# Performance work log

Measured on AMD Instinct MI355X. Metric: run time of the kernel, lower is better.

Reference implementation:

```python
import jax, jax.numpy as jnp
import numpy as np

HID, NL, NH, DH, FF = 768, 12, 12, 64, 3072
VOCAB, MAXPOS = 30522, 512
T_ELE, T_ROLE = 17, 7
B, L = 16, 256
LN_EPS = 1e-12


def _layernorm(x, g, b):
    mu = x.mean(-1, keepdims=True)
    var = ((x - mu) ** 2).mean(-1, keepdims=True)
    return (x - mu) / jnp.sqrt(var + LN_EPS) * g + b


def _bert(datas, word_emb, pos_emb, type_emb, emb_ln_g, emb_ln_b,
          Wq, bq, Wk, bk, Wv, bv, Wo, bo, ln1_g, ln1_b,
          W1, b1, W2, b2, ln2_g, ln2_b):
    Bv, Lv = datas.shape
    x = word_emb[datas] + pos_emb[:Lv][None] + type_emb[0][None, None]
    x = _layernorm(x, emb_ln_g, emb_ln_b)
    for i in range(NL):  # loop over fixed layer count, not data dims
        q = (x @ Wq[i] + bq[i]).reshape(Bv, Lv, NH, DH)
        k = (x @ Wk[i] + bk[i]).reshape(Bv, Lv, NH, DH)
        v = (x @ Wv[i] + bv[i]).reshape(Bv, Lv, NH, DH)
        att = jax.nn.softmax(jnp.einsum('bqhd,bkhd->bhqk', q, k) / jnp.sqrt(jnp.float32(DH)), axis=-1)
        ctx = jnp.einsum('bhqk,bkhd->bqhd', att, v).reshape(Bv, Lv, HID)
        x = _layernorm(x + ctx @ Wo[i] + bo[i], ln1_g[i], ln1_b[i])
        h = jax.nn.gelu(x @ W1[i] + b1[i], approximate=False)
        x = _layernorm(x + h @ W2[i] + b2[i], ln2_g[i], ln2_b[i])
    return x


def _crf_llh(em, tags, mask, start, end, trans):
    # torchcrf CRF.forward with batch_first=True, reduction='sum'
    Bv, Lv, T = em.shape
    bidx = jnp.arange(Bv)
    em_t = jnp.transpose(em, (1, 0, 2))        # [L,B,T]
    tags_t = tags.T.astype(jnp.int32)          # [L,B]
    mask_t = mask.T.astype(em.dtype)           # [L,B]
    # numerator: score of gold path
    score = start[tags_t[0]] + em_t[0][bidx, tags_t[0]]
    def num_step(s, xs):
        e_t, tg, tp, m = xs
        return s + m * (trans[tp, tg] + e_t[bidx, tg]), None
    score, _ = jax.lax.scan(num_step, score, (em_t[1:], tags_t[1:], tags_t[:-1], mask_t[1:]))
    last_idx = (mask_t.sum(0) - 1).astype(jnp.int32)
    num = score + end[tags[bidx, last_idx]]
    # denominator: forward algorithm (log-sum-exp semiring)
    alpha = start[None] + em_t[0]              # [B,T]
    def den_step(a, xs):
        e_t, m = xs
        nxt = jax.nn.logsumexp(a[:, :, None] + trans[None] + e_t[:, None, :], axis=1)
        return jnp.where(m[:, None] > 0, nxt, a), None
    alpha, _ = jax.lax.scan(den_step, alpha, (em_t[1:], mask_t[1:]))
    den = jax.nn.logsumexp(alpha + end[None], axis=1)
    return jnp.sum(num - den)


def _crf_decode(em, start, end, trans):
    # torchcrf CRF.decode without mask -> full-length Viterbi
    Bv = em.shape[0]
    bidx = jnp.arange(Bv)
    em_t = jnp.transpose(em, (1, 0, 2))        # [L,B,T]
    alpha = start[None] + em_t[0]
    def fwd(a, e_t):
        sc = a[:, :, None] + trans[None]       # [B,T_prev,T_cur]
        return jnp.max(sc, axis=1) + e_t, jnp.argmax(sc, axis=1)
    alpha, hist = jax.lax.scan(fwd, alpha, em_t[1:])   # hist [L-1,B,T]
    last = jnp.argmax(alpha + end[None], axis=1)
    def back(cur, h):
        prev = h[bidx, cur]
        return prev, prev
    _, ys = jax.lax.scan(back, last, hist, reverse=True)  # ys[t] = tag at pos t
    return jnp.concatenate([ys, last[None]], axis=0).T    # [B,L]


def setup_inputs() -> dict:
    key = jax.random.key(0)
    ks = iter(jax.random.split(key, 64))
    n = lambda shape: jax.random.normal(next(ks), shape, dtype=jnp.float32) * 0.02
    inp = {
        'datas': jax.random.randint(next(ks), (B, L), 0, VOCAB, dtype=jnp.int32),
        'ele_labels': jax.random.randint(next(ks), (B, L), 0, T_ELE, dtype=jnp.int32),
        'role_labels': jax.random.randint(next(ks), (B, L), 0, T_ROLE, dtype=jnp.int32),
        'seq_mask': jnp.ones((B, L), dtype=bool),
        'word_emb': n((VOCAB, HID)), 'pos_emb': n((MAXPOS, HID)), 'type_emb': n((2, HID)),
        'emb_ln_g': jnp.ones((HID,)), 'emb_ln_b': jnp.zeros((HID,)),
        'Wq': n((NL, HID, HID)), 'bq': jnp.zeros((NL, HID)),
        'Wk': n((NL, HID, HID)), 'bk': jnp.zeros((NL, HID)),
        'Wv': n((NL, HID, HID)), 'bv': jnp.zeros((NL, HID)),
        'Wo': n((NL, HID, HID)), 'bo': jnp.zeros((NL, HID)),
        'ln1_g': jnp.ones((NL, HID)), 'ln1_b': jnp.zeros((NL, HID)),
        'W1': n((NL, HID, FF)), 'b1': jnp.zeros((NL, FF)),
        'W2': n((NL, FF, HID)), 'b2': jnp.zeros((NL, HID)),
        'ln2_g': jnp.ones((NL, HID)), 'ln2_b': jnp.zeros((NL, HID)),
        'W_ele': n((HID, T_ELE)), 'b_ele': jnp.zeros((T_ELE,)),
        'W_role': n((HID, T_ROLE)), 'b_role': jnp.zeros((T_ROLE,)),
        'ele_start': n((T_ELE,)), 'ele_end': n((T_ELE,)), 'ele_trans': n((T_ELE, T_ELE)),
        'role_start': n((T_ROLE,)), 'role_end': n((T_ROLE,)), 'role_trans': n((T_ROLE, T_ROLE)),
    }
    return inp


def reference(datas, ele_labels, role_labels, seq_mask,
              word_emb, pos_emb, type_emb, emb_ln_g, emb_ln_b,
              Wq, bq, Wk, bk, Wv, bv, Wo, bo, ln1_g, ln1_b,
              W1, b1, W2, b2, ln2_g, ln2_b,
              W_ele, b_ele, W_role, b_role,
              ele_start, ele_end, ele_trans, role_start, role_end, role_trans):
    wemb = _bert(datas, word_emb, pos_emb, type_emb, emb_ln_g, emb_ln_b,
                 Wq, bq, Wk, bk, Wv, bv, Wo, bo, ln1_g, ln1_b,
                 W1, b1, W2, b2, ln2_g, ln2_b)
    ele_em = wemb @ W_ele + b_ele
    role_em = wemb @ W_role + b_role
    mask = seq_mask.astype(jnp.float32)
    ele_llh = _crf_llh(ele_em, ele_labels, mask, ele_start, ele_end, ele_trans)
    role_llh = _crf_llh(role_em, role_labels, mask, role_start, role_end, role_trans)
    loss = -ele_llh - role_llh
    ele_dec = _crf_decode(ele_em, ele_start, ele_end, ele_trans)
    role_dec = _crf_decode(role_em, role_start, role_end, role_trans)
    return loss, ele_dec, role_dec
```

## Files before the change

kernel.cpp:

```cpp
#include <hip/hip_runtime.h>
#include <stdint.h>
#include <math.h>

typedef _Float16 f16;
typedef _Float16 f16x8 __attribute__((ext_vector_type(8)));
typedef float f32x4 __attribute__((ext_vector_type(4)));

#define LO_SCALE 2048.0f
#define INV_LO_SCALE (1.0f/2048.0f)
#define LOG2E 1.4426950408889634f
#define MFMA16(a, b, c) __builtin_amdgcn_mfma_f32_16x16x32_f16(a, b, c, 0, 0, 0)

__device__ __forceinline__ void split1(float x, f16 &hi, f16 &lo) {
    f16 h = (f16)x;
    hi = h;
    lo = (f16)((x - (float)h) * LO_SCALE);
}

__device__ __forceinline__ float fexp2(float x) {
#if __has_builtin(__builtin_amdgcn_exp2f)
    return __builtin_amdgcn_exp2f(x);
#else
    return exp2f(x);
#endif
}
__device__ __forceinline__ float flog2(float x) {
#if __has_builtin(__builtin_amdgcn_logf)
    return __builtin_amdgcn_logf(x);
#else
    return log2f(x);
#endif
}

#define GLOAD16(g, l) __builtin_amdgcn_global_load_lds( \
    (const __attribute__((address_space(1))) void*)(g), \
    (__attribute__((address_space(3))) void*)(l), 16, 0, 0)

#define RAW_BARRIER() do { \
    __builtin_amdgcn_s_barrier(); \
    asm volatile("" ::: "memory"); \
    __builtin_amdgcn_sched_barrier(0); \
} while (0)

__device__ __forceinline__ void swz_decode(int &mi, int &ni)
{
    const int NN = gridDim.y;
    int s = blockIdx.x + blockIdx.y * gridDim.x;
    const int c = s & 7;
    const int idx = s >> 3;
    const int mchunk = gridDim.x >> 3;
    const int md = idx / NN;
    mi = c * mchunk + md;
    ni = idx - md * NN;
}

template<int EPI>
__device__ __forceinline__ void epi_write(float val, int row, int col, int N,
                                          float* __restrict__ C,
                                          f16* __restrict__ Oh, f16* __restrict__ Ol,
                                          f16* __restrict__ X2h, f16* __restrict__ X2l,
                                          f16* __restrict__ X3h, f16* __restrict__ X3l)
{
    if constexpr (EPI == 0) {
        C[(size_t)row * N + col] = val;
    } else if constexpr (EPI == 1) {
        float ge = 0.5f * val * (1.0f + erff(val * 0.70710678118654752440f));
        f16 hi, lo;
        split1(ge, hi, lo);
        size_t o = (size_t)row * N + col;
        Oh[o] = hi;
        Ol[o] = lo;
    } else {
        int sect = col >= 1536 ? 2 : (col >= 768 ? 1 : 0);
        int cc = col - sect * 768;
        int hd = cc >> 6;
        int d = cc & 63;
        int bh = (row >> 8) * 12 + hd;
        int lt = row & 255;
        f16 hi, lo;
        split1(val, hi, lo);
        if (sect == 0) {
            size_t o = ((size_t)bh * 256 + lt) * 64 + d;
            Oh[o] = hi; Ol[o] = lo;
        } else if (sect == 1) {
            size_t o = ((size_t)bh * 256 + lt) * 64 + d;
            X2h[o] = hi; X2l[o] = lo;
        } else {
            size_t o = ((size_t)bh * 64 + d) * 256 + lt;
            X3h[o] = hi; X3l[o] = lo;
        }
    }
}

template<int EPI>
__global__ __launch_bounds__(256, 2)
void gemm128(const f16* __restrict__ Ah, const f16* __restrict__ Al,
             const f16* __restrict__ Bh, const f16* __restrict__ Bl,
             const float* __restrict__ bias, float* __restrict__ C,
             f16* __restrict__ Oh, f16* __restrict__ Ol,
             f16* __restrict__ X2h, f16* __restrict__ X2l,
             f16* __restrict__ X3h, f16* __restrict__ X3l, int K, int N)
{
    __shared__ f16 smem[2][16384];

    int mi, ni;
    swz_decode(mi, ni);
    const int m0 = mi * 128;
    const int n0 = ni * 128;

    const int tid = threadIdx.x;
    const int lane = tid & 63;
    const int w = tid >> 6;
    const int l15 = lane & 15;
    const int lg = lane >> 4;

    f32x4 accm[4][4];
    f32x4 accc[4][4];
#pragma unroll
    for (int i = 0; i < 4; ++i)
#pragma unroll
        for (int j = 0; j < 4; ++j) {
            accm[i][j] = (f32x4){0.f, 0.f, 0.f, 0.f};
            accc[i][j] = (f32x4){0.f, 0.f, 0.f, 0.f};
        }

    const f16* gA0 = Ah + (size_t)(m0 + w * 32 + l15) * K + lg * 8;
    const f16* gA1 = gA0 + 16 * (size_t)K;
    const f16* gAl0 = Al + (size_t)(m0 + w * 32 + l15) * K + lg * 8;
    const f16* gAl1 = gAl0 + 16 * (size_t)K;
    const f16* gB0 = Bh + (size_t)(n0 + w * 32 + l15) * K + lg * 8;
    const f16* gB1 = gB0 + 16 * (size_t)K;
    const f16* gBl0 = Bl + (size_t)(n0 + w * 32 + l15) * K + lg * 8;
    const f16* gBl1 = gBl0 + 16 * (size_t)K;
    const int ldsb0 = w * 1024;
    const int ldsb1 = w * 1024 + 512;

    const int nt = K >> 5;

#define STAGE(buf, k0)                                   \
    {                                                    \
        f16* sb = &smem[buf][0];                         \
        GLOAD16(gA0 + (k0), sb + ldsb0);                 \
        GLOAD16(gA1 + (k0), sb + ldsb1);                 \
        GLOAD16(gAl0 + (k0), sb + 4096 + ldsb0);         \
        GLOAD16(gAl1 + (k0), sb + 4096 + ldsb1);         \
        GLOAD16(gB0 + (k0), sb + 8192 + ldsb0);          \
        GLOAD16(gB1 + (k0), sb + 8192 + ldsb1);          \
        GLOAD16(gBl0 + (k0), sb + 12288 + ldsb0);        \
        GLOAD16(gBl1 + (k0), sb + 12288 + ldsb1);        \
    }

    STAGE(0, 0);

    const int fro = lg * 128 + l15 * 8;
    const int wrg = (w >> 1) * 4;
    const int wcg = (w & 1) * 4;

    int cur = 0;
    for (int t = 0; t < nt; ++t) {
        if (t + 1 < nt) {
            STAGE(cur ^ 1, (t + 1) * 32);
            asm volatile("s_waitcnt vmcnt(8)" ::: "memory");
        } else {
            asm volatile("s_waitcnt vmcnt(0)" ::: "memory");
        }
        RAW_BARRIER();

        const f16* sb = &smem[cur][0];
        f16x8 fbh[4], fbl[4];
#pragma unroll
        for (int ni2 = 0; ni2 < 4; ++ni2) {
            int offb = 8192 + (wcg + ni2) * 512 + fro;
            fbh[ni2] = *(const f16x8*)(sb + offb);
            fbl[ni2] = *(const f16x8*)(sb + offb + 4096);
        }
#pragma unroll
        for (int mi2 = 0; mi2 < 4; ++mi2) {
            int offa = (wrg + mi2) * 512 + fro;
            f16x8 fah = *(const f16x8*)(sb + offa);
            f16x8 fal = *(const f16x8*)(sb + offa + 4096);
            __builtin_amdgcn_s_setprio(1);
#pragma unroll
            for (int ni2 = 0; ni2 < 4; ++ni2) {
                accm[mi2][ni2] = MFMA16(fah, fbh[ni2], accm[mi2][ni2]);
                accc[mi2][ni2] = MFMA16(fah, fbl[ni2], accc[mi2][ni2]);
                accc[mi2][ni2] = MFMA16(fal, fbh[ni2], accc[mi2][ni2]);
            }
            __builtin_amdgcn_s_setprio(0);
        }

        asm volatile("s_waitcnt lgkmcnt(0)" ::: "memory");
        RAW_BARRIER();
        cur ^= 1;
    }
#undef STAGE

    const int wr = (w >> 1) * 64;
    const int wc = (w & 1) * 64;
#pragma unroll
    for (int mi2 = 0; mi2 < 4; ++mi2) {
        int row = m0 + wr + mi2 * 16 + lg * 4;
#pragma unroll
        for (int ni2 = 0; ni2 < 4; ++ni2) {
            int col = n0 + wc + ni2 * 16 + l15;
            float bv = bias[col];
#pragma unroll
            for (int j = 0; j < 4; ++j) {
                float val = accm[mi2][ni2][j] + accc[mi2][ni2][j] * INV_LO_SCALE + bv;
                epi_write<EPI>(val, row + j, col, N, C, Oh, Ol, X2h, X2l, X3h, X3l);
            }
        }
    }
}

template<int EPI>
__global__ __launch_bounds__(256, 3)
void gemm_t64c(const f16* __restrict__ Ah, const f16* __restrict__ Al,
               const f16* __restrict__ Bh, const f16* __restrict__ Bl,
               const float* __restrict__ bias, float* __restrict__ C,
               f16* __restrict__ Oh, f16* __restrict__ Ol,
               f16* __restrict__ X2h, f16* __restrict__ X2l,
               f16* __restrict__ X3h, f16* __restrict__ X3l, int K, int N)
{
    __shared__ f16 smem[2][12288];

    int mi, ni;
    swz_decode(mi, ni);
    const int m0 = mi * 128;
    const int n0 = ni * 64;

    const int tid = threadIdx.x;
    const int lane = tid & 63;
    const int w = tid >> 6;
    const int l15 = lane & 15;
    const int lg = lane >> 4;

    f32x4 accm[4][2];
    f32x4 accc[4][2];
#pragma unroll
    for (int i = 0; i < 4; ++i)
#pragma unroll
        for (int j = 0; j < 2; ++j) {
            accm[i][j] = (f32x4){0.f, 0.f, 0.f, 0.f};
            accc[i][j] = (f32x4){0.f, 0.f, 0.f, 0.f};
        }

    const f16* gA0 = Ah + (size_t)(m0 + w * 32 + l15) * K + lg * 8;
    const f16* gA1 = gA0 + 16 * (size_t)K;
    const f16* gAl0 = Al + (size_t)(m0 + w * 32 + l15) * K + lg * 8;
    const f16* gAl1 = gAl0 + 16 * (size_t)K;
    const f16* gB0 = Bh + (size_t)(n0 + w * 16 + l15) * K + lg * 8;
    const f16* gBl0 = Bl + (size_t)(n0 + w * 16 + l15) * K + lg * 8;

    const int nt = K >> 5;

#define STAGEB(buf, k0)                                  \
    {                                                    \
        f16* sb = &smem[buf][0];                         \
        GLOAD16(gA0 + (k0), sb + w * 1024);              \
        GLOAD16(gA1 + (k0), sb + w * 1024 + 512);        \
        GLOAD16(gAl0 + (k0), sb + 4096 + w * 1024);      \
        GLOAD16(gAl1 + (k0), sb + 4096 + w * 1024 + 512);\
        GLOAD16(gB0 + (k0), sb + 8192 + w * 512);        \
        GLOAD16(gBl0 + (k0), sb + 10240 + w * 512);      \
    }

    STAGEB(0, 0);

    const int fro = lg * 128 + l15 * 8;
    const int wrg = (w >> 1) * 4;
    const int wcg = (w & 1) * 2;

    int cur = 0;
    for (int t = 0; t < nt; ++t) {
        if (t + 1 < nt) {
            STAGEB(cur ^ 1, (t + 1) * 32);
            asm volatile("s_waitcnt vmcnt(6)" ::: "memory");
        } else {
            asm volatile("s_waitcnt vmcnt(0)" ::: "memory");
        }
        RAW_BARRIER();

        const f16* sb = &smem[cur][0];
        f16x8 fbh[2], fbl[2];
#pragma unroll
        for (int ni2 = 0; ni2 < 2; ++ni2) {
            int offb = 8192 + (wcg + ni2) * 512 + fro;
            fbh[ni2] = *(const f16x8*)(sb + offb);
            fbl[ni2] = *(const f16x8*)(sb + offb + 2048);
        }
#pragma unroll
        for (int mi2 = 0; mi2 < 4; ++mi2) {
            int offa = (wrg + mi2) * 512 + fro;
            f16x8 fah = *(const f16x8*)(sb + offa);
            f16x8 fal = *(const f16x8*)(sb + offa + 4096);
            __builtin_amdgcn_s_setprio(1);
#pragma unroll
            for (int ni2 = 0; ni2 < 2; ++ni2) {
                accm[mi2][ni2] = MFMA16(fah, fbh[ni2], accm[mi2][ni2]);
                accc[mi2][ni2] = MFMA16(fah, fbl[ni2], accc[mi2][ni2]);
                accc[mi2][ni2] = MFMA16(fal, fbh[ni2], accc[mi2][ni2]);
            }
            __builtin_amdgcn_s_setprio(0);
        }

        asm volatile("s_waitcnt lgkmcnt(0)" ::: "memory");
        RAW_BARRIER();
        cur ^= 1;
    }
#undef STAGEB

    const int wr = (w >> 1) * 64;
    const int wc = (w & 1) * 32;
#pragma unroll
    for (int mi2 = 0; mi2 < 4; ++mi2) {
        int row = m0 + wr + mi2 * 16 + lg * 4;
#pragma unroll
        for (int ni2 = 0; ni2 < 2; ++ni2) {
            int col = n0 + wc + ni2 * 16 + l15;
            float bv = bias[col];
#pragma unroll
            for (int j = 0; j < 4; ++j) {
                float val = accm[mi2][ni2][j] + accc[mi2][ni2][j] * INV_LO_SCALE + bv;
                epi_write<EPI>(val, row + j, col, N, C, Oh, Ol, X2h, X2l, X3h, X3l);
            }
        }
    }
}

__global__ __launch_bounds__(256, 1)
void attn_mfma_kernel(const f16* __restrict__ Qh, const f16* __restrict__ Ql,
                      const f16* __restrict__ Kh, const f16* __restrict__ Kl,
                      const f16* __restrict__ Vth, const f16* __restrict__ Vtl,
                      f16* __restrict__ ch, f16* __restrict__ cl)
{
    __shared__ f16 sKh[256 * 72];
    __shared__ f16 sKl[256 * 72];
    __shared__ f16 sVh[64 * 264];
    __shared__ f16 sVl[64 * 264];
    __shared__ f16 sPh[4][1280];
    __shared__ f16 sPl[4][1280];

    const int bh = blockIdx.x >> 1;
    const int qbase = (blockIdx.x & 1) * 128;
    const int b = bh / 12;
    const int h = bh % 12;
    const int tid = threadIdx.x;
    const int w = tid >> 6;
    const int l = tid & 63;
    const int l15 = l & 15;
    const int lg = l >> 4;

    {
        const f16* gKh = Kh + (size_t)bh * 16384;
        const f16* gKl = Kl + (size_t)bh * 16384;
#pragma unroll
        for (int i = 0; i < 8; ++i) {
            int c = tid + i * 256;
            int off = (c >> 3) * 72 + (c & 7) * 8;
            *(f16x8*)(sKh + off) = *(const f16x8*)(gKh + c * 8);
            *(f16x8*)(sKl + off) = *(const f16x8*)(gKl + c * 8);
        }
        const f16* gVh = Vth + (size_t)bh * 16384;
        const f16* gVl = Vtl + (size_t)bh * 16384;
#pragma unroll
        for (int i = 0; i < 8; ++i) {
            int c = tid + i * 256;
            int off = (c >> 5) * 264 + (c & 31) * 8;
            *(f16x8*)(sVh + off) = *(const f16x8*)(gVh + c * 8);
            *(f16x8*)(sVl + off) = *(const f16x8*)(gVl + c * 8);
        }
    }
    __syncthreads();

    f16x8 qfh[2][2], qfl[2][2];
#pragma unroll
    for (int mt = 0; mt < 2; ++mt) {
        int qr = qbase + w * 32 + mt * 16 + l15;
        size_t qo = ((size_t)bh * 256 + qr) * 64 + lg * 8;
        qfh[mt][0] = *(const f16x8*)(Qh + qo);
        qfh[mt][1] = *(const f16x8*)(Qh + qo + 32);
        qfl[mt][0] = *(const f16x8*)(Ql + qo);
        qfl[mt][1] = *(const f16x8*)(Ql + qo + 32);
    }

    f32x4 S[2][16];
#pragma unroll
    for (int nt = 0; nt < 16; ++nt) {
        int kr = nt * 16 + l15;
        int kaddr = kr * 72 + lg * 8;
        f16x8 kh0 = *(const f16x8*)(sKh + kaddr);
        f16x8 kh1 = *(const f16x8*)(sKh + kaddr + 32);
        f16x8 kl0 = *(const f16x8*)(sKl + kaddr);
        f16x8 kl1 = *(const f16x8*)(sKl + kaddr + 32);
#pragma unroll
        for (int mt = 0; mt < 2; ++mt) {
            f32x4 am = (f32x4){0.f, 0.f, 0.f, 0.f};
            f32x4 ac = (f32x4){0.f, 0.f, 0.f, 0.f};
            am = MFMA16(qfh[mt][0], kh0, am);
            am = MFMA16(qfh[mt][1], kh1, am);
            ac = MFMA16(qfh[mt][0], kl0, ac);
            ac = MFMA16(qfh[mt][1], kl1, ac);
            ac = MFMA16(qfl[mt][0], kh0, ac);
            ac = MFMA16(qfl[mt][1], kh1, ac);
            S[mt][nt] = (am + ac * INV_LO_SCALE) * 0.125f;
        }
    }

#pragma unroll
    for (int mt = 0; mt < 2; ++mt)
#pragma unroll
        for (int j = 0; j < 4; ++j) {
            float m = S[mt][0][j];
#pragma unroll
            for (int nt = 1; nt < 16; ++nt) m = fmaxf(m, S[mt][nt][j]);
            m = fmaxf(m, __shfl_xor(m, 1));
            m = fmaxf(m, __shfl_xor(m, 2));
            m = fmaxf(m, __shfl_xor(m, 4));
            m = fmaxf(m, __shfl_xor(m, 8));
            float s = 0.f;
#pragma unroll
            for (int nt = 0; nt < 16; ++nt) {
                float e = fexp2((S[mt][nt][j] - m) * LOG2E);
                S[mt][nt][j] = e;
                s += e;
            }
            s += __shfl_xor(s, 1);
            s += __shfl_xor(s, 2);
            s += __shfl_xor(s, 4);
            s += __shfl_xor(s, 8);
            float inv = 1.0f / s;
#pragma unroll
            for (int nt = 0; nt < 16; ++nt) S[mt][nt][j] *= inv;
        }

    f32x4 Ohh[2][4], Occ[2][4];
#pragma unroll
    for (int mt = 0; mt < 2; ++mt)
#pragma unroll
        for (int dt = 0; dt < 4; ++dt) {
            Ohh[mt][dt] = (f32x4){0.f, 0.f, 0.f, 0.f};
            Occ[mt][dt] = (f32x4){0.f, 0.f, 0.f, 0.f};
        }

    f16* pbh = &sPh[w][0];
    f16* pbl = &sPl[w][0];
#pragma unroll
    for (int kp = 0; kp < 8; ++kp) {
#pragma unroll
        for (int mt = 0; mt < 2; ++mt)
#pragma unroll
            for (int n2 = 0; n2 < 2; ++n2) {
                int nt = kp * 2 + n2;
#pragma unroll
                for (int j = 0; j < 4; ++j) {
                    int prow = mt * 16 + lg * 4 + j;
                    int pcol = n2 * 16 + l15;
                    f16 hi, lo;
                    split1(S[mt][nt][j], hi, lo);
                    pbh[prow * 40 + pcol] = hi;
                    pbl[prow * 40 + pcol] = lo;
                }
            }
        __builtin_amdgcn_wave_barrier();
#pragma unroll
        for (int mt = 0; mt < 2; ++mt) {
            int paddr = (mt * 16 + l15) * 40 + lg * 8;
            f16x8 ph = *(const f16x8*)(pbh + paddr);
            f16x8 pl = *(const f16x8*)(pbl + paddr);
#pragma unroll
            for (int dt = 0; dt < 4; ++dt) {
                int vaddr = (dt * 16 + l15) * 264 + kp * 32 + lg * 8;
                f16x8 vh = *(const f16x8*)(sVh + vaddr);
                f16x8 vl = *(const f16x8*)(sVl + vaddr);
                Ohh[mt][dt] = MFMA16(ph, vh, Ohh[mt][dt]);
                Occ[mt][dt] = MFMA16(ph, vl, Occ[mt][dt]);
                Occ[mt][dt] = MFMA16(pl, vh, Occ[mt][dt]);
            }
        }
        __builtin_amdgcn_wave_barrier();
    }

#pragma unroll
    for (int mt = 0; mt < 2; ++mt)
#pragma unroll
        for (int dt = 0; dt < 4; ++dt) {
            f32x4 o = Ohh[mt][dt] + Occ[mt][dt] * INV_LO_SCALE;
#pragma unroll
            for (int j = 0; j < 4; ++j) {
                int q = qbase + w * 32 + mt * 16 + lg * 4 + j;
                int d = dt * 16 + l15;
                size_t off = ((size_t)(b * 256 + q)) * 768 + h * 64 + d;
                f16 hi, lo;
                split1(o[j], hi, lo);
                ch[off] = hi;
                cl[off] = lo;
            }
        }
}

__device__ __forceinline__ void tsplit_tile(const float* __restrict__ W,
                                            f16* __restrict__ Th, f16* __restrict__ Tl,
                                            int K, int N, int kb, int nb, int tid,
                                            float (*tile)[33])
{
    const int k0 = kb * 32;
    const int n0 = nb * 32;
    const int r = tid >> 3;
    const int c4 = (tid & 7) * 4;
    float4 v = *(const float4*)&W[(size_t)(k0 + r) * N + n0 + c4];
    tile[r][c4 + 0] = v.x; tile[r][c4 + 1] = v.y;
    tile[r][c4 + 2] = v.z; tile[r][c4 + 3] = v.w;
    __syncthreads();
    f16 hs[4], ls[4];
#pragma unroll
    for (int j = 0; j < 4; ++j) split1(tile[c4 + j][r], hs[j], ls[j]);
    size_t o = (size_t)(n0 + r) * K + k0 + c4;
    Th[o + 0] = hs[0]; Th[o + 1] = hs[1]; Th[o + 2] = hs[2]; Th[o + 3] = hs[3];
    Tl[o + 0] = ls[0]; Tl[o + 1] = ls[1]; Tl[o + 2] = ls[2]; Tl[o + 3] = ls[3];
}

__global__ void tsplit_all_kernel(const float* __restrict__ Wq, const float* __restrict__ Wk,
                                  const float* __restrict__ Wv, const float* __restrict__ Wo,
                                  const float* __restrict__ W1, const float* __restrict__ W2,
                                  f16* __restrict__ qkvh, f16* __restrict__ qkvl,
                                  f16* __restrict__ woh, f16* __restrict__ wol,
                                  f16* __restrict__ w1h, f16* __restrict__ w1l,
                                  f16* __restrict__ w2h, f16* __restrict__ w2l)
{
    __shared__ float tile[32][33];
    const int tid = threadIdx.x;
    int bid = blockIdx.x;
    if (bid < 576) {
        tsplit_tile(Wq, qkvh, qkvl, 768, 768, bid % 24, bid / 24, tid, tile);
    } else if (bid < 1152) {
        bid -= 576;
        tsplit_tile(Wk, qkvh + 768 * 768, qkvl + 768 * 768, 768, 768, bid % 24, bid / 24, tid, tile);
    } else if (bid < 1728) {
        bid -= 1152;
        tsplit_tile(Wv, qkvh + 2 * 768 * 768, qkvl + 2 * 768 * 768, 768, 768, bid % 24, bid / 24, tid, tile);
    } else if (bid < 2304) {
        bid -= 1728;
        tsplit_tile(Wo, woh, wol, 768, 768, bid % 24, bid / 24, tid, tile);
    } else if (bid < 4608) {
        bid -= 2304;
        tsplit_tile(W1, w1h, w1l, 768, 3072, bid % 24, bid / 24, tid, tile);
    } else {
        bid -= 4608;
        tsplit_tile(W2, w2h, w2l, 3072, 768, bid % 96, bid / 96, tid, tile);
    }
}

__global__ void pack_qkv_bias_kernel(const float* __restrict__ bq, const float* __restrict__ bk,
                                     const float* __restrict__ bv, float* __restrict__ qkvb)
{
    const int i = blockIdx.x;
    const int tid = threadIdx.x;
    for (int c = tid; c < 768; c += 256) {
        qkvb[i * 2304 + c]        = bq[i * 768 + c];
        qkvb[i * 2304 + 768 + c]  = bk[i * 768 + c];
        qkvb[i * 2304 + 1536 + c] = bv[i * 768 + c];
    }
}

__device__ void ln_emit(float* vals, float* red, const float* __restrict__ g,
                        const float* __restrict__ be, float* xout,
                        f16* oh, f16* ol, size_t base, int tid)
{
    float s = vals[tid] + vals[tid + 256] + vals[tid + 512];
    red[tid] = s;
    __syncthreads();
    for (int st = 128; st > 0; st >>= 1) { if (tid < st) red[tid] += red[tid + st]; __syncthreads(); }
    float mu = red[0] * (1.0f / 768.0f);
    __syncthreads();
    float d0 = vals[tid] - mu, d1 = vals[tid + 256] - mu, d2 = vals[tid + 512] - mu;
    red[tid] = d0 * d0 + d1 * d1 + d2 * d2;
    __syncthreads();
    for (int st = 128; st > 0; st >>= 1) { if (tid < st) red[tid] += red[tid + st]; __syncthreads(); }
    float var = red[0] * (1.0f / 768.0f);
    float rstd = 1.0f / sqrtf(var + 1e-12f);
    __syncthreads();
    for (int c = tid; c < 768; c += 256) {
        float o = (vals[c] - mu) * rstd * g[c] + be[c];
        if (xout) xout[base + c] = o;
        f16 hi, lo;
        split1(o, hi, lo);
        oh[base + c] = hi;
        ol[base + c] = lo;
    }
}

__global__ void embed_ln_kernel(const int* __restrict__ datas, const float* __restrict__ wemb,
                                const float* __restrict__ pemb, const float* __restrict__ temb,
                                const float* __restrict__ g, const float* __restrict__ be,
                                float* __restrict__ x, f16* __restrict__ xh, f16* __restrict__ xl)
{
    __shared__ float vals[768];
    __shared__ float red[256];
    const int i = blockIdx.x;
    const int tid = threadIdx.x;
    const int l = i & 255;
    const int widx = datas[i];
    for (int c = tid; c < 768; c += 256)
        vals[c] = wemb[(size_t)widx * 768 + c] + pemb[(size_t)l * 768 + c] + temb[c];
    __syncthreads();
    ln_emit(vals, red, g, be, x, xh, xl, (size_t)i * 768, tid);
}

__global__ void res_ln_kernel(float* __restrict__ x, const float* __restrict__ y,
                              const float* __restrict__ g, const float* __restrict__ be,
                              f16* __restrict__ xh, f16* __restrict__ xl)
{
    __shared__ float vals[768];
    __shared__ float red[256];
    const int i = blockIdx.x;
    const int tid = threadIdx.x;
    const size_t base = (size_t)i * 768;
    for (int c = tid; c < 768; c += 256) vals[c] = x[base + c] + y[base + c];
    __syncthreads();
    ln_emit(vals, red, g, be, x, xh, xl, base, tid);
}

__global__ void head_kernel(const float* __restrict__ X, const float* __restrict__ Wh,
                            const float* __restrict__ bh, float* __restrict__ out, int T)
{
    __shared__ float xs[768];
    __shared__ double part[8][32];
    const int i = blockIdx.x;
    const int tid = threadIdx.x;
    for (int c = tid; c < 768; c += 256) xs[c] = X[(size_t)i * 768 + c];
    __syncthreads();
    const int p = tid >> 5;
    const int tg = tid & 31;
    if (tg < T) {
        double a = 0;
        for (int d = p * 96; d < p * 96 + 96; ++d)
            a += (double)xs[d] * (double)Wh[d * T + tg];
        part[p][tg] = a;
    }
    __syncthreads();
    if (tid < T) {
        double s = 0;
        for (int pp = 0; pp < 8; ++pp) s += part[pp][tid];
        out[(size_t)i * T + tid] = (float)(s + (double)bh[tid]);
    }
}

__global__ void crf_num_kernel(const float* __restrict__ em, const int* __restrict__ labels,
                               const float* __restrict__ start, const float* __restrict__ endv,
                               const float* __restrict__ trans, float* __restrict__ num, int T)
{
    __shared__ double red[256];
    const int b = blockIdx.x;
    const int tid = threadIdx.x;
    const int tag = labels[b * 256 + tid];
    float v;
    if (tid == 0) {
        v = start[tag] + em[(size_t)(b * 256) * T + tag];
    } else {
        int pt = labels[b * 256 + tid - 1];
        v = trans[pt * T + tag] + em[(size_t)(b * 256 + tid) * T + tag];
    }
    red[tid] = (double)v;
    __syncthreads();
    for (int st = 128; st > 0; st >>= 1) { if (tid < st) red[tid] += red[tid + st]; __syncthreads(); }
    if (tid == 0) num[b] = (float)(red[0] + (double)endv[labels[b * 256 + 255]]);
}

template<int T>
__global__ void crf_scan_kernel(const float* __restrict__ emG, const float* __restrict__ start,
                                const float* __restrict__ endv, const float* __restrict__ trans,
                                float* __restrict__ den, float* __restrict__ tagOut)
{
    __shared__ float ems[256 * T];
    __shared__ float albuf[32];
    __shared__ unsigned char hist[255 * T + 1];
    const int b = blockIdx.x;
    const bool vit = (blockIdx.y == 1);
    const int c = threadIdx.x;

    for (int idx = c; idx < 256 * T; idx += 64)
        ems[idx] = emG[(size_t)b * 256 * T + idx];
    float trc[T];
#pragma unroll
    for (int p = 0; p < T; ++p) trc[p] = (c < T) ? trans[p * T + c] : 0.f;
    const float ec = (c < T) ? endv[c] : -1e30f;
    __syncthreads();

    float alpha = (c < T) ? (start[c] + ems[c]) : -1e30f;

    if (!vit) {
        for (int t = 1; t < 256; ++t) {
            if (c < T) albuf[c] = alpha;
            __builtin_amdgcn_wave_barrier();
            float a[T];
            float m = -1e30f;
#pragma unroll
            for (int p = 0; p < T; ++p) { a[p] = albuf[p] + trc[p]; m = fmaxf(m, a[p]); }
            float s = 0.f;
#pragma unroll
            for (int p = 0; p < T; ++p) s += fexp2((a[p] - m) * LOG2E);
            float na = m + flog2(s) * 0.6931471805599453f + ems[t * T + c];
            __builtin_amdgcn_wave_barrier();
            if (c < T) alpha = na;
        }
        if (c < T) albuf[c] = alpha + ec;
        __builtin_amdgcn_wave_barrier();
        if (c == 0) {
            float m = -1e30f;
            for (int p = 0; p < T; ++p) m = fmaxf(m, albuf[p]);
            float s = 0.f;
            for (int p = 0; p < T; ++p) s += fexp2((albuf[p] - m) * LOG2E);
            den[b] = m + flog2(s) * 0.6931471805599453f;
        }
    } else {
        for (int t = 1; t < 256; ++t) {
            if (c < T) albuf[c] = alpha;
            __builtin_amdgcn_wave_barrier();
            float best = albuf[0] + trc[0];
            int arg = 0;
#pragma unroll
            for (int p = 1; p < T; ++p) {
                float v2 = albuf[p] + trc[p];
                if (v2 > best) { best = v2; arg = p; }
            }
            __builtin_amdgcn_wave_barrier();
            if (c < T) {
                alpha = best + ems[t * T + c];
                hist[(t - 1) * T + c] = (unsigned char)arg;
            }
        }
        if (c < T) albuf[c] = alpha + ec;
        __builtin_amdgcn_wave_barrier();
        if (c == 0) {
            float bv = albuf[0];
            int cur = 0;
            for (int p = 1; p < T; ++p) {
                if (albuf[p] > bv) { bv = albuf[p]; cur = p; }
            }
            tagOut[b * 256 + 255] = (float)cur;
            for (int t = 254; t >= 0; --t) {
                cur = hist[t * T + cur];
                tagOut[b * 256 + t] = (float)cur;
            }
        }
    }
}

__global__ void loss_kernel(const float* __restrict__ num, const float* __restrict__ den,
                            float* __restrict__ out)
{
    __shared__ double red[32];
    const int tid = threadIdx.x;
    red[tid] = (double)num[tid] - (double)den[tid];
    __syncthreads();
    for (int st = 16; st > 0; st >>= 1) { if (tid < st) red[tid] += red[tid + st]; __syncthreads(); }
    if (tid == 0) out[0] = (float)(-red[0]);
}

extern "C" void kernel_launch(void* const* d_in, const int* in_sizes, int n_in,
                              void* d_out, int out_size, void* d_ws, size_t ws_size,
                              hipStream_t stream)
{
    (void)in_sizes; (void)n_in; (void)out_size; (void)ws_size;
    const int* datas       = (const int*)d_in[0];
    const int* ele_labels  = (const int*)d_in[1];
    const int* role_labels = (const int*)d_in[2];
    const float* word_emb = (const float*)d_in[4];
    const float* pos_emb  = (const float*)d_in[5];
    const float* type_emb = (const float*)d_in[6];
    const float* emb_g = (const float*)d_in[7];
    const float* emb_b = (const float*)d_in[8];
    const float* Wq = (const float*)d_in[9];  const float* bq = (const float*)d_in[10];
    const float* Wk = (const float*)d_in[11]; const float* bk = (const float*)d_in[12];
    const float* Wv = (const float*)d_in[13]; const float* bv = (const float*)d_in[14];
    const float* Wo = (const float*)d_in[15]; const float* bo = (const float*)d_in[16];
    const float* ln1g = (const float*)d_in[17]; const float* ln1b = (const float*)d_in[18];
    const float* W1 = (const float*)d_in[19]; const float* b1 = (const float*)d_in[20];
    const float* W2 = (const float*)d_in[21]; const float* b2 = (const float*)d_in[22];
    const float* ln2g = (const float*)d_in[23]; const float* ln2b = (const float*)d_in[24];
    const float* W_ele = (const float*)d_in[25]; const float* b_ele = (const float*)d_in[26];
    const float* W_role = (const float*)d_in[27]; const float* b_role = (const float*)d_in[28];
    const float* ele_start = (const float*)d_in[29];
    const float* ele_end   = (const float*)d_in[30];
    const float* ele_trans = (const float*)d_in[31];
    const float* role_start = (const float*)d_in[32];
    const float* role_end   = (const float*)d_in[33];
    const float* role_trans = (const float*)d_in[34];
    float* out = (float*)d_out;

    uint8_t* ws = (uint8_t*)d_ws;
    float* x      = (float*)(ws + 0x0000000);
    f16* xh       = (f16*)  (ws + 0x0C00000);
    f16* xl       = (f16*)  (ws + 0x1200000);
    f16* Qh       = (f16*)  (ws + 0x1800000);
    f16* Ql       = (f16*)  (ws + 0x1E00000);
    f16* Kh       = (f16*)  (ws + 0x2400000);
    f16* Kl       = (f16*)  (ws + 0x2A00000);
    f16* Vth      = (f16*)  (ws + 0x3000000);
    f16* Vtl      = (f16*)  (ws + 0x3600000);
    f16* ctxh     = (f16*)  (ws + 0x3C00000);
    f16* ctxl     = (f16*)  (ws + 0x4200000);
    float* rbuf   = (float*)(ws + 0x4800000);
    f16* hh       = (f16*)  (ws + 0x1800000);
    f16* hl       = (f16*)  (ws + 0x3000000);
    f16* wqkv_h   = (f16*)  (ws + 0x5400000);
    f16* wqkv_l   = (f16*)  (ws + 0x5760000);
    f16* wo_h     = (f16*)  (ws + 0x5AC0000);
    f16* wo_l     = (f16*)  (ws + 0x5BE0000);
    f16* w1_h     = (f16*)  (ws + 0x5D00000);
    f16* w1_l     = (f16*)  (ws + 0x6180000);
    f16* w2_h     = (f16*)  (ws + 0x6600000);
    f16* w2_l     = (f16*)  (ws + 0x6A80000);
    float* qkvb   = (float*)(ws + 0x6F00000);
    float* ele_em = (float*)(ws + 0x6F20000);
    float* role_em= (float*)(ws + 0x6F70000);
    float* numb   = (float*)(ws + 0x6FC0000);
    float* denb   = (float*)(ws + 0x6FC0100);

    pack_qkv_bias_kernel<<<12, 256, 0, stream>>>(bq, bk, bv, qkvb);
    embed_ln_kernel<<<4096, 256, 0, stream>>>(datas, word_emb, pos_emb, type_emb,
                                              emb_g, emb_b, x, xh, xl);

    for (int i = 0; i < 12; ++i) {
        const size_t o768 = (size_t)i * 768 * 768;
        const size_t o3072 = (size_t)i * 768 * 3072;
        tsplit_all_kernel<<<6912, 256, 0, stream>>>(Wq + o768, Wk + o768, Wv + o768, Wo + o768,
                                                    W1 + o3072, W2 + o3072,
                                                    wqkv_h, wqkv_l, wo_h, wo_l,
                                                    w1_h, w1_l, w2_h, w2_l);
        gemm128<2><<<dim3(32, 18), 256, 0, stream>>>(xh, xl, wqkv_h, wqkv_l,
                                                     qkvb + i * 2304, nullptr,
                                                     Qh, Ql, Kh, Kl, Vth, Vtl, 768, 2304);
        attn_mfma_kernel<<<384, 256, 0, stream>>>(Qh, Ql, Kh, Kl, Vth, Vtl, ctxh, ctxl);
        gemm_t64c<0><<<dim3(32, 12), 256, 0, stream>>>(ctxh, ctxl, wo_h, wo_l,
                                                       bo + i * 768, rbuf, nullptr, nullptr,
                                                       nullptr, nullptr, nullptr, nullptr, 768, 768);
        res_ln_kernel<<<4096, 256, 0, stream>>>(x, rbuf, ln1g + i * 768, ln1b + i * 768, xh, xl);
        gemm128<1><<<dim3(32, 24), 256, 0, stream>>>(xh, xl, w1_h, w1_l,
                                                     b1 + i * 3072, nullptr, hh, hl,
                                                     nullptr, nullptr, nullptr, nullptr, 768, 3072);
        gemm_t64c<0><<<dim3(32, 12), 256, 0, stream>>>(hh, hl, w2_h, w2_l,
                                                       b2 + i * 768, rbuf, nullptr, nullptr,
                                                       nullptr, nullptr, nullptr, nullptr, 3072, 768);
        res_ln_kernel<<<4096, 256, 0, stream>>>(x, rbuf, ln2g + i * 768, ln2b + i * 768, xh, xl);
    }

    head_kernel<<<4096, 256, 0, stream>>>(x, W_ele, b_ele, ele_em, 17);
    head_kernel<<<4096, 256, 0, stream>>>(x, W_role, b_role, role_em, 7);

    crf_num_kernel<<<16, 256, 0, stream>>>(ele_em, ele_labels, ele_start, ele_end, ele_trans, numb, 17);
    crf_num_kernel<<<16, 256, 0, stream>>>(role_em, role_labels, role_start, role_end, role_trans, numb + 16, 7);
    crf_scan_kernel<17><<<dim3(16, 2), 64, 0, stream>>>(ele_em, ele_start, ele_end, ele_trans, denb, out + 1);
    crf_scan_kernel<7><<<dim3(16, 2), 64, 0, stream>>>(role_em, role_start, role_end, role_trans, denb + 16, out + 1 + 4096);
    loss_kernel<<<1, 32, 0, stream>>>(numb, denb, out);
}
```

Measured before the change: 5.826 ms.

## Replace 128x128 GEMM with 256x128 8-wave triple-buffered interleaved-load kernel

Replaces the 4-wave 128x128 double-buffered GEMM used for the QKV and FFN1 projections with an 8-wave 256x128 tile kernel. It uses a three-stage LDS ring, prefetching two K-steps ahead, and spreads the global-to-LDS stage loads across the MFMA sub-iterations with per-subtile barriers. The aim is better latency hiding and more reuse of each B tile. In exchange it uses more LDS and allows only one block per CU. It also halves the grid, which may leave CUs underfilled on a 256-CU part, and adds many more barriers.

```diff
diff --git a/kernel.cpp b/kernel.cpp
--- a/kernel.cpp
+++ b/kernel.cpp
@@ -93,20 +93,20 @@
 }
 
 template<int EPI>
-__global__ __launch_bounds__(256, 2)
-void gemm128(const f16* __restrict__ Ah, const f16* __restrict__ Al,
-             const f16* __restrict__ Bh, const f16* __restrict__ Bl,
-             const float* __restrict__ bias, float* __restrict__ C,
-             f16* __restrict__ Oh, f16* __restrict__ Ol,
-             f16* __restrict__ X2h, f16* __restrict__ X2l,
-             f16* __restrict__ X3h, f16* __restrict__ X3l, int K, int N)
-{
-    __shared__ f16 smem[2][16384];
-
-    int mi, ni;
-    swz_decode(mi, ni);
-    const int m0 = mi * 128;
-    const int n0 = ni * 128;
+__global__ __launch_bounds__(512, 1)
+void gemm8p(const f16* __restrict__ Ah, const f16* __restrict__ Al,
+            const f16* __restrict__ Bh, const f16* __restrict__ Bl,
+            const float* __restrict__ bias, float* __restrict__ C,
+            f16* __restrict__ Oh, f16* __restrict__ Ol,
+            f16* __restrict__ X2h, f16* __restrict__ X2l,
+            f16* __restrict__ X3h, f16* __restrict__ X3l, int K, int N)
+{
+    __shared__ f16 smem[3][24576];
+
+    int mi_, ni_;
+    swz_decode(mi_, ni_);
+    const int m0 = mi_ * 256;
+    const int n0 = ni_ * 128;
 
     const int tid = threadIdx.x;
     const int lane = tid & 63;
@@ -128,72 +128,80 @@
     const f16* gA1 = gA0 + 16 * (size_t)K;
     const f16* gAl0 = Al + (size_t)(m0 + w * 32 + l15) * K + lg * 8;
     const f16* gAl1 = gAl0 + 16 * (size_t)K;
-    const f16* gB0 = Bh + (size_t)(n0 + w * 32 + l15) * K + lg * 8;
-    const f16* gB1 = gB0 + 16 * (size_t)K;
-    const f16* gBl0 = Bl + (size_t)(n0 + w * 32 + l15) * K + lg * 8;
-    const f16* gBl1 = gBl0 + 16 * (size_t)K;
-    const int ldsb0 = w * 1024;
-    const int ldsb1 = w * 1024 + 512;
+    const f16* gB0 = Bh + (size_t)(n0 + w * 16 + l15) * K + lg * 8;
+    const f16* gBl0 = Bl + (size_t)(n0 + w * 16 + l15) * K + lg * 8;
 
     const int nt = K >> 5;
 
-#define STAGE(buf, k0)                                   \
-    {                                                    \
-        f16* sb = &smem[buf][0];                         \
-        GLOAD16(gA0 + (k0), sb + ldsb0);                 \
-        GLOAD16(gA1 + (k0), sb + ldsb1);                 \
-        GLOAD16(gAl0 + (k0), sb + 4096 + ldsb0);         \
-        GLOAD16(gAl1 + (k0), sb + 4096 + ldsb1);         \
-        GLOAD16(gB0 + (k0), sb + 8192 + ldsb0);          \
-        GLOAD16(gB1 + (k0), sb + 8192 + ldsb1);          \
-        GLOAD16(gBl0 + (k0), sb + 12288 + ldsb0);        \
-        GLOAD16(gBl1 + (k0), sb + 12288 + ldsb1);        \
-    }
-
-    STAGE(0, 0);
+#define SA_HI(buf, k0) { f16* sb = &smem[buf][0]; \
+    GLOAD16(gA0 + (k0), sb + w * 1024); \
+    GLOAD16(gA1 + (k0), sb + w * 1024 + 512); }
+#define SA_LO(buf, k0) { f16* sb = &smem[buf][0]; \
+    GLOAD16(gAl0 + (k0), sb + 8192 + w * 1024); \
+    GLOAD16(gAl1 + (k0), sb + 8192 + w * 1024 + 512); }
+#define SB_HL(buf, k0) { f16* sb = &smem[buf][0]; \
+    GLOAD16(gB0 + (k0), sb + 16384 + w * 512); \
+    GLOAD16(gBl0 + (k0), sb + 20480 + w * 512); }
+
+    SA_HI(0, 0); SA_LO(0, 0); SB_HL(0, 0);
+    if (nt > 1) { SA_HI(1, 32); SA_LO(1, 32); SB_HL(1, 32); }
 
     const int fro = lg * 128 + l15 * 8;
-    const int wrg = (w >> 1) * 4;
-    const int wcg = (w & 1) * 4;
-
-    int cur = 0;
+    const int wag = (w >> 1) * 4;
+    const int wbg = (w & 1) * 4;
+
+    int bt = 0;
     for (int t = 0; t < nt; ++t) {
         if (t + 1 < nt) {
-            STAGE(cur ^ 1, (t + 1) * 32);
-            asm volatile("s_waitcnt vmcnt(8)" ::: "memory");
+            asm volatile("s_waitcnt vmcnt(6)" ::: "memory");
         } else {
             asm volatile("s_waitcnt vmcnt(0)" ::: "memory");
         }
         RAW_BARRIER();
 
-        const f16* sb = &smem[cur][0];
+        const f16* sb = &smem[bt][0];
+        int bs = bt + 2; if (bs >= 3) bs -= 3;
+        const bool doStage = (t + 2 < nt);
+        const int k2 = (t + 2) * 32;
+
         f16x8 fbh[4], fbl[4];
 #pragma unroll
-        for (int ni2 = 0; ni2 < 4; ++ni2) {
-            int offb = 8192 + (wcg + ni2) * 512 + fro;
-            fbh[ni2] = *(const f16x8*)(sb + offb);
-            fbl[ni2] = *(const f16x8*)(sb + offb + 4096);
-        }
-#pragma unroll
-        for (int mi2 = 0; mi2 < 4; ++mi2) {
-            int offa = (wrg + mi2) * 512 + fro;
+        for (int mt = 0; mt < 4; ++mt) {
+            if (doStage) {
+                if (mt == 0) { SA_HI(bs, k2); }
+                else if (mt == 1) { SA_LO(bs, k2); }
+                else if (mt == 2) { SB_HL(bs, k2); }
+            }
+            if (mt == 0) {
+#pragma unroll
+                for (int ni2 = 0; ni2 < 4; ++ni2) {
+                    int offb = 16384 + (wbg + ni2) * 512 + fro;
+                    fbh[ni2] = *(const f16x8*)(sb + offb);
+                    fbl[ni2] = *(const f16x8*)(sb + offb + 4096);
+                }
+            }
+            int offa = (wag + mt) * 512 + fro;
             f16x8 fah = *(const f16x8*)(sb + offa);
-            f16x8 fal = *(const f16x8*)(sb + offa + 4096);
+            f16x8 fal = *(const f16x8*)(sb + offa + 8192);
+
+            __builtin_amdgcn_s_barrier();
+            asm volatile("s_waitcnt lgkmcnt(0)" ::: "memory");
+            __builtin_amdgcn_sched_barrier(0);
             __builtin_amdgcn_s_setprio(1);
 #pragma unroll
             for (int ni2 = 0; ni2 < 4; ++ni2) {
-                accm[mi2][ni2] = MFMA16(fah, fbh[ni2], accm[mi2][ni2]);
-                accc[mi2][ni2] = MFMA16(fah, fbl[ni2], accc[mi2][ni2]);
-                accc[mi2][ni2] = MFMA16(fal, fbh[ni2], accc[mi2][ni2]);
+                accm[mt][ni2] = MFMA16(fah, fbh[ni2], accm[mt][ni2]);
+                accc[mt][ni2] = MFMA16(fah, fbl[ni2], accc[mt][ni2]);
+                accc[mt][ni2] = MFMA16(fal, fbh[ni2], accc[mt][ni2]);
             }
             __builtin_amdgcn_s_setprio(0);
-        }
-
-        asm volatile("s_waitcnt lgkmcnt(0)" ::: "memory");
-        RAW_BARRIER();
-        cur ^= 1;
-    }
-#undef STAGE
+            __builtin_amdgcn_s_barrier();
+        }
+        bt = bt + 1; if (bt >= 3) bt = 0;
+    }
+#undef SA_HI
+#undef SA_LO
+#undef SB_HL
 
     const int wr = (w >> 1) * 64;
     const int wc = (w & 1) * 64;
@@ -829,17 +837,17 @@
                                                     W1 + o3072, W2 + o3072,
                                                     wqkv_h, wqkv_l, wo_h, wo_l,
                                                     w1_h, w1_l, w2_h, w2_l);
-        gemm128<2><<<dim3(32, 18), 256, 0, stream>>>(xh, xl, wqkv_h, wqkv_l,
-                                                     qkvb + i * 2304, nullptr,
-                                                     Qh, Ql, Kh, Kl, Vth, Vtl, 768, 2304);
+        gemm8p<2><<<dim3(16, 18), 512, 0, stream>>>(xh, xl, wqkv_h, wqkv_l,
+                                                    qkvb + i * 2304, nullptr,
+                                                    Qh, Ql, Kh, Kl, Vth, Vtl, 768, 2304);
         attn_mfma_kernel<<<384, 256, 0, stream>>>(Qh, Ql, Kh, Kl, Vth, Vtl, ctxh, ctxl);
         gemm_t64c<0><<<dim3(32, 12), 256, 0, stream>>>(ctxh, ctxl, wo_h, wo_l,
                                                        bo + i * 768, rbuf, nullptr, nullptr,
                                                        nullptr, nullptr, nullptr, nullptr, 768, 768);
         res_ln_kernel<<<4096, 256, 0, stream>>>(x, rbuf, ln1g + i * 768, ln1b + i * 768, xh, xl);
-        gemm128<1><<<dim3(32, 24), 256, 0, stream>>>(xh, xl, w1_h, w1_l,
-                                                     b1 + i * 3072, nullptr, hh, hl,
-                                                     nullptr, nullptr, nullptr, nullptr, 768, 3072);
+        gemm8p<1><<<dim3(16, 24), 512, 0, stream>>>(xh, xl, w1_h, w1_l,
+                                                    b1 + i * 3072, nullptr, hh, hl,
+                                                    nullptr, nullptr, nullptr, nullptr, 768, 3072);
         gemm_t64c<0><<<dim3(32, 12), 256, 0, stream>>>(hh, hl, w2_h, w2_l,
                                                        b2 + i * 768, rbuf, nullptr, nullptr,
                                                        nullptr, nullptr, nullptr, nullptr, 3072, 768);
```

Measured after the change: 5.885 ms. Within noise of the previous version (+1.0%).
